# Performance work log

Hardware: AMD Instinct MI355X
Metric: run time of the kernel (lower is better)

## Reference

```python
import jax, jax.numpy as jnp
import numpy as np


def setup_inputs() -> dict:
    key = jax.random.key(0)
    k1, k2, k3, k4 = jax.random.split(key, 4)
    B, S, DIN, DOUT = 4, 4096, 512, 128
    x = jax.random.normal(k1, (B, S, DIN), dtype=jnp.float32)
    Wq = jax.random.normal(k2, (DIN, DOUT), dtype=jnp.float32) * 0.02
    Wk = jax.random.normal(k3, (DIN, DOUT), dtype=jnp.float32) * 0.02
    Wv = jax.random.normal(k4, (DIN, DOUT), dtype=jnp.float32) * 0.02
    return {"x": x, "Wq": Wq, "Wk": Wk, "Wv": Wv}


def reference(x, Wq, Wk, Wv):
    # x: [B, S, d_in]; projections (bias-free Linear)
    q = jnp.einsum('bsd,de->bse', x, Wq)  # [B, S, d_out]
    k = jnp.einsum('bsd,de->bse', x, Wk)
    v = jnp.einsum('bsd,de->bse', x, Wv)
    d_out = k.shape[-1]
    scores = jnp.einsum('bqe,bke->bqk', q, k) / jnp.sqrt(jnp.float32(d_out))  # [B, S, S]
    S = x.shape[1]
    causal = jnp.tril(jnp.ones((S, S), dtype=bool))  # True where attending allowed
    scores = jnp.where(causal[None], scores, jnp.float32(-jnp.inf))
    attn = jax.nn.softmax(scores, axis=-1)
    # dropout p=0.0 -> identity (eval mode)
    return jnp.einsum('bqk,bke->bqe', attn, v)  # [B, S, d_out]
```

## Files before the change

### kernel.cpp

```cpp
#include <hip/hip_runtime.h>

typedef __bf16 bf16x8 __attribute__((ext_vector_type(8)));
typedef float f32x4 __attribute__((ext_vector_type(4)));
typedef unsigned short u16;
typedef unsigned int u32;
typedef u16 u16x8 __attribute__((ext_vector_type(8)));
typedef u16 u16x4 __attribute__((ext_vector_type(4)));
typedef u32 u32x4 __attribute__((ext_vector_type(4)));

__device__ __forceinline__ u16 f2bf(float f) {
    u32 u = __builtin_bit_cast(u32, f);
    u += 0x7fffu + ((u >> 16) & 1u);
    return (u16)(u >> 16);
}
__device__ __forceinline__ float bf2f(u16 v) {
    return __builtin_bit_cast(float, (u32)v << 16);
}
__device__ __forceinline__ u32 cvtpk(float a, float b) {
    u32 d;
    asm("v_cvt_pk_bf16_f32 %0, %1, %2" : "=v"(d) : "v"(a), "v"(b));
    return d;
}
__device__ __forceinline__ f32x4 mfma16(u16x8 a, u16x8 b, f32x4 c) {
    return __builtin_amdgcn_mfma_f32_16x16x32_bf16(
        __builtin_bit_cast(bf16x8, a), __builtin_bit_cast(bf16x8, b), c, 0, 0, 0);
}

#define GLOAD16(SRC, DST)                                                     \
    __builtin_amdgcn_global_load_lds(                                         \
        (const __attribute__((address_space(1))) unsigned int*)(SRC),         \
        (__attribute__((address_space(3))) unsigned int*)(DST), 16, 0, 0)

__device__ __forceinline__ int ldsAddr(int r, int c) {
    return r * 128 + (((c >> 3) ^ (r & 7)) << 3) + (c & 7);
}

__global__ __launch_bounds__(256) void prep_all(
    const float* __restrict__ x,
    const float* __restrict__ Wq, const float* __restrict__ Wk,
    const float* __restrict__ Wv,
    u16* __restrict__ xf, u16* __restrict__ wf)
{
    __shared__ u16 T[16 * 512];
    const int t = threadIdx.x;
    if (blockIdx.x < 1024) {
        const int rb = blockIdx.x;
        const int row = t >> 4, colb = (t & 15) * 32;
        const float* src = x + (size_t)(rb * 16 + row) * 512 + colb;
        #pragma unroll
        for (int i = 0; i < 4; ++i) {
            float4 va = *(const float4*)(src + i * 8);
            float4 vb = *(const float4*)(src + i * 8 + 4);
            u16x8 v;
            v[0] = f2bf(va.x); v[1] = f2bf(va.y); v[2] = f2bf(va.z); v[3] = f2bf(va.w);
            v[4] = f2bf(vb.x); v[5] = f2bf(vb.y); v[6] = f2bf(vb.z); v[7] = f2bf(vb.w);
            int chunk = ((colb >> 3) + i) ^ (row & 7);
            *(u16x8*)&T[row * 512 + chunk * 8] = v;
        }
        __syncthreads();
        #pragma unroll
        for (int ii = 0; ii < 4; ++ii) {
            int flatF = ii * 256 + t;
            int ds = flatF >> 6, lane = flatF & 63;
            int l16 = lane & 15, g = lane >> 4;
            int chunk = (4 * ds + g) ^ (l16 & 7);
            u16x8 v = *(const u16x8*)&T[l16 * 512 + chunk * 8];
            *(u16x8*)&xf[(((size_t)rb * 16 + ds) * 64 + lane) * 8] = v;
        }
    } else {
        int flat = (blockIdx.x - 1024) * 256 + t;
        int widx = flat >> 13, rem = flat & 8191;
        int n = rem >> 10, ds = (rem >> 6) & 15, lane = rem & 63;
        int l16 = lane & 15, g = lane >> 4;
        const float* W = (widx == 0) ? Wq : (widx == 1 ? Wk : Wv);
        const float sc = (widx == 0) ? (0.08838834764831845f * 1.4426950408889634f) : 1.0f;
        u16x8 v;
        #pragma unroll
        for (int j = 0; j < 8; ++j)
            v[j] = f2bf(W[(size_t)(ds * 32 + 8 * g + j) * 128 + n * 16 + l16] * sc);
        *(u16x8*)&wf[(size_t)flat * 8] = v;
    }
}

__global__ __launch_bounds__(256, 3) void qkv2(
    const u16* __restrict__ xf, const u16* __restrict__ wf,
    u16* __restrict__ Qf, u16* __restrict__ Kf, u16* __restrict__ Vf)
{
    __shared__ u16 Wbuf[2][4096];
    __shared__ u16 T4[4][16 * 128];
    const int tid = threadIdx.x, lane = tid & 63, wid = tid >> 6;
    const int g = lane >> 4, l16 = lane & 15;
    const int widx = blockIdx.y;
    const int rbg = blockIdx.x * 4 + wid;
    const u16* WfB = wf + (size_t)widx * 65536;
    u16* T = T4[wid];

    GLOAD16(WfB + (size_t)((wid * 16 + 0) * 64 + lane) * 8,
            Wbuf[0] + (wid * 64 + lane) * 8);
    GLOAD16(WfB + (size_t)(((wid + 4) * 16 + 0) * 64 + lane) * 8,
            Wbuf[0] + ((wid + 4) * 64 + lane) * 8);

    const f32x4 fz = {0.f, 0.f, 0.f, 0.f};
    f32x4 acc[8];
    #pragma unroll
    for (int n = 0; n < 8; ++n) acc[n] = fz;

    u16x8 a_cur = *(const u16x8*)&xf[(((size_t)rbg * 16 + 0) * 64 + lane) * 8];
    __syncthreads();

    #pragma unroll 1
    for (int ds = 0; ds < 16; ++ds) {
        u16x8 a_next;
        if (ds + 1 < 16) {
            const int nds = ds + 1, bb = nds & 1;
            GLOAD16(WfB + (size_t)((wid * 16 + nds) * 64 + lane) * 8,
                    Wbuf[bb] + (wid * 64 + lane) * 8);
            GLOAD16(WfB + (size_t)(((wid + 4) * 16 + nds) * 64 + lane) * 8,
                    Wbuf[bb] + ((wid + 4) * 64 + lane) * 8);
            a_next = *(const u16x8*)&xf[(((size_t)rbg * 16 + nds) * 64 + lane) * 8];
        }
        const u16* Wl = Wbuf[ds & 1];
        #pragma unroll
        for (int n = 0; n < 8; ++n) {
            u16x8 b = *(const u16x8*)&Wl[(n * 64 + lane) * 8];
            acc[n] = mfma16(a_cur, b, acc[n]);
        }
        __syncthreads();
        if (ds + 1 < 16) a_cur = a_next;
    }

    #pragma unroll
    for (int n = 0; n < 8; ++n) {
        #pragma unroll
        for (int r = 0; r < 4; ++r)
            T[ldsAddr(4 * g + r, n * 16 + l16)] = f2bf(acc[n][r]);
    }
    if (widx < 2) {
        u16* dst = (widx == 0) ? Qf : Kf;
        #pragma unroll
        for (int ds = 0; ds < 4; ++ds) {
            int chunk = (4 * ds + g) ^ (l16 & 7);
            u16x8 v = *(const u16x8*)&T[l16 * 128 + chunk * 8];
            *(u16x8*)&dst[(((size_t)rbg * 4 + ds) * 64 + lane) * 8] = v;
        }
    } else {
        const int kb = rbg >> 2, ksel = (rbg >> 1) & 1, g0 = (rbg & 1) * 2;
        #pragma unroll
        for (int s = 0; s < 4; ++s) {
            int flat = s * 64 + lane;
            int e = flat >> 5, gg = (flat >> 4) & 1, l16p = flat & 15;
            u16x8 v;
            #pragma unroll
            for (int j = 0; j < 8; ++j)
                v[j] = T[ldsAddr(8 * gg + j, e * 16 + l16p)];
            *(u16x8*)&Vf[((((size_t)kb * 2 + ksel) * 8 + e) * 64
                          + (g0 + gg) * 16 + l16p) * 8] = v;
        }
    }
}

__global__ __launch_bounds__(256, 2) void attn6(
    const u16* __restrict__ Qf, const u16* __restrict__ Kf,
    const u16* __restrict__ Vf, float* __restrict__ out,
    u16* __restrict__ po, float* __restrict__ pml, int split)
{
    __shared__ u16 lds[2][16384];
    const int tid = threadIdx.x, lane = tid & 63, wid = tid >> 6;
    const int g = lane >> 4, l16 = lane & 15;

    int b, qb, c, u;
    if (split) {
        const int xcd = blockIdx.x & 7;
        b = xcd >> 1;
        int jb = 271 - ((xcd & 1) * 136 + (blockIdx.x >> 3));
        u = 0;
        while ((u + 1) * (u + 2) <= jb) ++u;
        int r = jb - u * (u + 1);
        int hi = (r >= u + 1) ? 1 : 0;
        qb = 2 * u + hi;
        c = r - hi * (u + 1);
    } else {
        b = blockIdx.x & 3;
        qb = blockIdx.x >> 2;
        c = 0; u = 0;
    }
    const int q0 = qb * 128 + wid * 32;
    const int k_lo = c * 256;
    const int k_hi = min(k_lo + (split ? 256 : 4096), qb * 128 + 128);
    const int nch = u + 1;
    const int wklen = q0 + 32;

    {
        const u16* src;
        if (wid < 2) src = Kf + (size_t)(b * 256 + (k_lo >> 4)) * 2048 + wid * 4096;
        else         src = Vf + (size_t)(b * 64 + (k_lo >> 6)) * 8192 + (wid - 2) * 4096;
        u16* dst = &lds[0][wid * 4096];
        #pragma unroll
        for (int j = 0; j < 8; ++j)
            GLOAD16(src + j * 512 + lane * 8, dst + j * 512);
    }
    const int rbq = b * 256 + qb * 8 + wid * 2;
    u16x8 qf0[4], qf1[4];
    #pragma unroll
    for (int ds = 0; ds < 4; ++ds) {
        qf0[ds] = *(const u16x8*)&Qf[(((size_t)rbq * 4 + ds) * 64 + lane) * 8];
        qf1[ds] = *(const u16x8*)&Qf[(((size_t)(rbq + 1) * 4 + ds) * 64 + lane) * 8];
    }

    const f32x4 fz = {0.f, 0.f, 0.f, 0.f};
    f32x4 o0[8], o1[8];
    #pragma unroll
    for (int e = 0; e < 8; ++e) { o0[e] = fz; o1[e] = fz; }
    float l0 = 0.f, l1 = 0.f;

    const int srcA = l16 + ((g & 1) << 5);
    const int srcB = srcA + 16;
    const bool hiSel = (g >= 2);

    __syncthreads();

    int bufsel = 0;
    for (int k0 = k_lo; k0 < k_hi; k0 += 64) {
        if (k0 + 64 < k_hi) {
            const u16* src;
            if (wid < 2) src = Kf + (size_t)(b * 256 + ((k0 + 64) >> 4)) * 2048 + wid * 4096;
            else         src = Vf + (size_t)(b * 64 + ((k0 + 64) >> 6)) * 8192 + (wid - 2) * 4096;
            u16* dst = &lds[bufsel ^ 1][wid * 4096];
            #pragma unroll
            for (int j = 0; j < 8; ++j)
                GLOAD16(src + j * 512 + lane * 8, dst + j * 512);
        }
        if (k0 < wklen) {
            const u16* Kl = &lds[bufsel][0];
            const u16* Vl = &lds[bufsel][8192];
            f32x4 st0[4], st1[4];
            __builtin_amdgcn_s_setprio(1);
            #pragma unroll
            for (int kt = 0; kt < 4; ++kt) {
                st0[kt] = fz; st1[kt] = fz;
                #pragma unroll
                for (int ds = 0; ds < 4; ++ds) {
                    u16x8 kf = *(const u16x8*)&Kl[(kt * 4 + ds) * 512 + lane * 8];
                    st0[kt] = mfma16(kf, qf0[ds], st0[kt]);
                    st1[kt] = mfma16(kf, qf1[ds], st1[kt]);
                }
            }
            __builtin_amdgcn_s_setprio(0);
            if (k0 + 63 > q0) {
                int qg = q0 + l16;
                #pragma unroll
                for (int kt = 0; kt < 4; ++kt)
                    #pragma unroll
                    for (int r = 0; r < 4; ++r)
                        if (k0 + kt * 16 + g * 4 + r > qg) st0[kt][r] = -1e30f;
            }
            if (k0 + 63 > q0 + 16) {
                int qg = q0 + 16 + l16;
                #pragma unroll
                for (int kt = 0; kt < 4; ++kt)
                    #pragma unroll
                    for (int r = 0; r < 4; ++r)
                        if (k0 + kt * 16 + g * 4 + r > qg) st1[kt][r] = -1e30f;
            }
            u32 pk0[4][2], pk1[4][2];
            #pragma unroll
            for (int kt = 0; kt < 4; ++kt) {
                float p0 = exp2f(st0[kt][0]), p1 = exp2f(st0[kt][1]);
                float p2 = exp2f(st0[kt][2]), p3 = exp2f(st0[kt][3]);
                l0 += (p0 + p1) + (p2 + p3);
                pk0[kt][0] = cvtpk(p0, p1);
                pk0[kt][1] = cvtpk(p2, p3);
                float q0v = exp2f(st1[kt][0]), q1v = exp2f(st1[kt][1]);
                float q2v = exp2f(st1[kt][2]), q3v = exp2f(st1[kt][3]);
                l1 += (q0v + q1v) + (q2v + q3v);
                pk1[kt][0] = cvtpk(q0v, q1v);
                pk1[kt][1] = cvtpk(q2v, q3v);
            }
            #pragma unroll
            for (int ksel = 0; ksel < 2; ++ksel) {
                u32 a0 = __shfl((int)pk0[2 * ksel][0], srcA), b0 = __shfl((int)pk0[2 * ksel + 1][0], srcA);
                u32 a1 = __shfl((int)pk0[2 * ksel][1], srcA), b1 = __shfl((int)pk0[2 * ksel + 1][1], srcA);
                u32 a2 = __shfl((int)pk0[2 * ksel][0], srcB), b2 = __shfl((int)pk0[2 * ksel + 1][0], srcB);
                u32 a3 = __shfl((int)pk0[2 * ksel][1], srcB), b3 = __shfl((int)pk0[2 * ksel + 1][1], srcB);
                u32x4 d0 = { hiSel ? b0 : a0, hiSel ? b1 : a1, hiSel ? b2 : a2, hiSel ? b3 : a3 };
                u16x8 pf0 = __builtin_bit_cast(u16x8, d0);
                u32 c0 = __shfl((int)pk1[2 * ksel][0], srcA), e0 = __shfl((int)pk1[2 * ksel + 1][0], srcA);
                u32 c1 = __shfl((int)pk1[2 * ksel][1], srcA), e1 = __shfl((int)pk1[2 * ksel + 1][1], srcA);
                u32 c2 = __shfl((int)pk1[2 * ksel][0], srcB), e2 = __shfl((int)pk1[2 * ksel + 1][0], srcB);
                u32 c3 = __shfl((int)pk1[2 * ksel][1], srcB), e3 = __shfl((int)pk1[2 * ksel + 1][1], srcB);
                u32x4 d1 = { hiSel ? e0 : c0, hiSel ? e1 : c1, hiSel ? e2 : c2, hiSel ? e3 : c3 };
                u16x8 pf1 = __builtin_bit_cast(u16x8, d1);
                __builtin_amdgcn_s_setprio(1);
                #pragma unroll
                for (int e = 0; e < 8; ++e) {
                    u16x8 vf = *(const u16x8*)&Vl[(ksel * 8 + e) * 512 + lane * 8];
                    o0[e] = mfma16(vf, pf0, o0[e]);
                    o1[e] = mfma16(vf, pf1, o1[e]);
                }
                __builtin_amdgcn_s_setprio(0);
            }
        }
        __syncthreads();
        bufsel ^= 1;
    }

    l0 += __shfl_xor(l0, 16); l0 += __shfl_xor(l0, 32);
    l1 += __shfl_xor(l1, 16); l1 += __shfl_xor(l1, 32);

    if (nch == 1) {
        float inv0 = 1.0f / l0, inv1 = 1.0f / l1;
        float* op0 = out + ((size_t)b * 4096 + q0 + l16) * 128;
        float* op1 = out + ((size_t)b * 4096 + q0 + 16 + l16) * 128;
        #pragma unroll
        for (int e = 0; e < 8; ++e) {
            f32x4 v0 = o0[e], v1 = o1[e];
            #pragma unroll
            for (int r = 0; r < 4; ++r) { v0[r] *= inv0; v1[r] *= inv1; }
            *(f32x4*)&op0[e * 16 + g * 4] = v0;
            *(f32x4*)&op1[e * 16 + g * 4] = v1;
        }
    } else {
        const int slot = b * 272 + u * (u + 1) + (qb & 1) * (u + 1) + c;
        u16* pp0 = po + ((size_t)slot * 128 + wid * 32 + l16) * 128;
        u16* pp1 = pp0 + 16 * 128;
        #pragma unroll
        for (int e = 0; e < 8; ++e) {
            u16x4 v0, v1;
            #pragma unroll
            for (int r = 0; r < 4; ++r) { v0[r] = f2bf(o0[e][r]); v1[r] = f2bf(o1[e][r]); }
            *(u16x4*)&pp0[e * 16 + g * 4] = v0;
            *(u16x4*)&pp1[e * 16 + g * 4] = v1;
        }
        if (g == 0) {
            pml[(size_t)slot * 128 + wid * 32 + l16] = l0;
            pml[(size_t)slot * 128 + wid * 32 + 16 + l16] = l1;
        }
    }
}

__global__ __launch_bounds__(256) void merge6(
    const u16* __restrict__ po, const float* __restrict__ pml,
    float* __restrict__ out)
{
    int gid = blockIdx.x * 256 + threadIdx.x;
    int colg = gid & 31;
    int rowid = gid >> 5;
    int b = rowid / 3840;
    int rr = rowid - b * 3840;
    int qb = (rr >> 7) + 2;
    int qr = rr & 127;
    int u = qb >> 1;
    int nch = u + 1;
    int slot0 = b * 272 + u * (u + 1) + (qb & 1) * (u + 1);

    float den = 0.f;
    f32x4 num = {0.f, 0.f, 0.f, 0.f};
    #pragma unroll 1
    for (int cc = 0; cc < nch; ++cc) {
        den += pml[(size_t)(slot0 + cc) * 128 + qr];
        u16x4 pv = *(const u16x4*)&po[((size_t)(slot0 + cc) * 128 + qr) * 128 + colg * 4];
        #pragma unroll
        for (int j = 0; j < 4; ++j) num[j] += bf2f(pv[j]);
    }
    float inv = 1.0f / den;
    f32x4 res = { num[0] * inv, num[1] * inv, num[2] * inv, num[3] * inv };
    *(f32x4*)&out[((size_t)b * 4096 + qb * 128 + qr) * 128 + colg * 4] = res;
}

extern "C" void kernel_launch(void* const* d_in, const int* in_sizes, int n_in,
                              void* d_out, int out_size, void* d_ws, size_t ws_size,
                              hipStream_t stream) {
    (void)in_sizes; (void)n_in; (void)out_size;
    const float* x  = (const float*)d_in[0];
    const float* Wq = (const float*)d_in[1];
    const float* Wk = (const float*)d_in[2];
    const float* Wv = (const float*)d_in[3];
    float* out = (float*)d_out;

    u16* Qf = (u16*)d_ws;
    u16* Kf = Qf + 2097152;
    u16* Vf = Kf + 2097152;
    u16* xf = Vf + 2097152;
    u16* wf = xf + 8388608;
    u16* po = xf;
    float* pml = (float*)(po + (size_t)1088 * 128 * 128);

    const size_t fixed_b = (size_t)3 * 2097152 * 2;
    const size_t part_b  = (size_t)1088 * 128 * (128 * 2 + 4);
    const int split = (ws_size >= fixed_b + part_b) ? 1 : 0;

    prep_all<<<1120, 256, 0, stream>>>(x, Wq, Wk, Wv, xf, wf);
    qkv2<<<dim3(256, 3), 256, 0, stream>>>(xf, wf, Qf, Kf, Vf);
    attn6<<<split ? 1088 : 128, 256, 0, stream>>>(Qf, Kf, Vf, out, po, pml, split);
    if (split) merge6<<<1920, 256, 0, stream>>>(po, pml, out);
}
```

Before: 79.29 us.

## Triple-buffer K/V tiles in attention with two-ahead prefetch and partial vmcnt waits

```diff
diff --git a/kernel.cpp b/kernel.cpp
--- a/kernel.cpp
+++ b/kernel.cpp
@@ -159,14 +159,16 @@
     }
 }
 
-__global__ __launch_bounds__(256, 2) void attn6(
+__global__ __launch_bounds__(256, 2) void attn8(
     const u16* __restrict__ Qf, const u16* __restrict__ Kf,
     const u16* __restrict__ Vf, float* __restrict__ out,
     u16* __restrict__ po, float* __restrict__ pml, int split)
 {
-    __shared__ u16 lds[2][16384];
+    __shared__ u16 lds[3][16384];
+    __shared__ u16 ldspad[8192];
     const int tid = threadIdx.x, lane = tid & 63, wid = tid >> 6;
     const int g = lane >> 4, l16 = lane & 15;
+    if (split == -12345) ldspad[tid] = 0;
 
     int b, qb, c, u;
     if (split) {
@@ -189,15 +191,26 @@
     const int k_hi = min(k_lo + (split ? 256 : 4096), qb * 128 + 128);
     const int nch = u + 1;
     const int wklen = q0 + 32;
+    const int nt = (k_hi - k_lo) >> 6;
 
     {
-        const u16* src;
-        if (wid < 2) src = Kf + (size_t)(b * 256 + (k_lo >> 4)) * 2048 + wid * 4096;
-        else         src = Vf + (size_t)(b * 64 + (k_lo >> 6)) * 8192 + (wid - 2) * 4096;
-        u16* dst = &lds[0][wid * 4096];
+        const u16* src0;
+        if (wid < 2) src0 = Kf + (size_t)(b * 256 + (k_lo >> 4)) * 2048 + wid * 4096;
+        else         src0 = Vf + (size_t)(b * 64 + (k_lo >> 6)) * 8192 + (wid - 2) * 4096;
+        u16* dst0 = &lds[0][wid * 4096];
         #pragma unroll
         for (int j = 0; j < 8; ++j)
-            GLOAD16(src + j * 512 + lane * 8, dst + j * 512);
+            GLOAD16(src0 + j * 512 + lane * 8, dst0 + j * 512);
+        if (nt > 1) {
+            const int k1 = k_lo + 64;
+            const u16* src1;
+            if (wid < 2) src1 = Kf + (size_t)(b * 256 + (k1 >> 4)) * 2048 + wid * 4096;
+            else         src1 = Vf + (size_t)(b * 64 + (k1 >> 6)) * 8192 + (wid - 2) * 4096;
+            u16* dst1 = &lds[1][wid * 4096];
+            #pragma unroll
+            for (int j = 0; j < 8; ++j)
+                GLOAD16(src1 + j * 512 + lane * 8, dst1 + j * 512);
+        }
     }
     const int rbq = b * 256 + qb * 8 + wid * 2;
     u16x8 qf0[4], qf1[4];
@@ -219,20 +232,25 @@
 
     __syncthreads();
 
-    int bufsel = 0;
-    for (int k0 = k_lo; k0 < k_hi; k0 += 64) {
-        if (k0 + 64 < k_hi) {
+    int bi = 0;
+    #pragma unroll 1
+    for (int it = 0; it < nt; ++it) {
+        const int k0 = k_lo + (it << 6);
+        const bool pf = (it + 2 < nt);
+        if (pf) {
+            const int kn = k0 + 128;
+            int pi = bi + 2; if (pi >= 3) pi -= 3;
             const u16* src;
-            if (wid < 2) src = Kf + (size_t)(b * 256 + ((k0 + 64) >> 4)) * 2048 + wid * 4096;
-            else         src = Vf + (size_t)(b * 64 + ((k0 + 64) >> 6)) * 8192 + (wid - 2) * 4096;
-            u16* dst = &lds[bufsel ^ 1][wid * 4096];
+            if (wid < 2) src = Kf + (size_t)(b * 256 + (kn >> 4)) * 2048 + wid * 4096;
+            else         src = Vf + (size_t)(b * 64 + (kn >> 6)) * 8192 + (wid - 2) * 4096;
+            u16* dst = &lds[pi][wid * 4096];
             #pragma unroll
             for (int j = 0; j < 8; ++j)
                 GLOAD16(src + j * 512 + lane * 8, dst + j * 512);
         }
         if (k0 < wklen) {
-            const u16* Kl = &lds[bufsel][0];
-            const u16* Vl = &lds[bufsel][8192];
+            const u16* Kl = &lds[bi][0];
+            const u16* Vl = &lds[bi][8192];
             f32x4 st0[4], st1[4];
             __builtin_amdgcn_s_setprio(1);
             #pragma unroll
@@ -300,8 +318,14 @@
                 __builtin_amdgcn_s_setprio(0);
             }
         }
-        __syncthreads();
-        bufsel ^= 1;
+        if (pf) {
+            asm volatile("s_waitcnt vmcnt(8) lgkmcnt(0)" ::: "memory");
+        } else {
+            asm volatile("s_waitcnt vmcnt(0) lgkmcnt(0)" ::: "memory");
+        }
+        __builtin_amdgcn_s_barrier();
+        __builtin_amdgcn_sched_barrier(0);
+        bi = (bi == 2) ? 0 : bi + 1;
     }
 
     l0 += __shfl_xor(l0, 16); l0 += __shfl_xor(l0, 32);
@@ -391,6 +415,6 @@
 
     prep_all<<<1120, 256, 0, stream>>>(x, Wq, Wk, Wv, xf, wf);
     qkv2<<<dim3(256, 3), 256, 0, stream>>>(xf, wf, Qf, Kf, Vf);
-    attn6<<<split ? 1088 : 128, 256, 0, stream>>>(Qf, Kf, Vf, out, po, pml, split);
+    attn8<<<split ? 1088 : 128, 256, 0, stream>>>(Qf, Kf, Vf, out, po, pml, split);
     if (split) merge6<<<1920, 256, 0, stream>>>(po, pml, out);
 }
```

New measurement: 101.2 us. +27.6%, slower.

## Enlarge attention query tile to 256 rows per block with 64 per wave

Applied to the files above, without the earlier changes.

```diff
diff --git a/kernel.cpp b/kernel.cpp
--- a/kernel.cpp
+++ b/kernel.cpp
@@ -159,7 +159,7 @@
     }
 }
 
-__global__ __launch_bounds__(256, 2) void attn6(
+__global__ __launch_bounds__(256, 2) void attn11(
     const u16* __restrict__ Qf, const u16* __restrict__ Kf,
     const u16* __restrict__ Vf, float* __restrict__ out,
     u16* __restrict__ po, float* __restrict__ pml, int split)
@@ -168,27 +168,29 @@
     const int tid = threadIdx.x, lane = tid & 63, wid = tid >> 6;
     const int g = lane >> 4, l16 = lane & 15;
 
-    int b, qb, c, u;
+    int b, qb, c, nch, slot;
     if (split) {
         const int xcd = blockIdx.x & 7;
         b = xcd >> 1;
-        int jb = 271 - ((xcd & 1) * 136 + (blockIdx.x >> 3));
-        u = 0;
-        while ((u + 1) * (u + 2) <= jb) ++u;
-        int r = jb - u * (u + 1);
-        int hi = (r >= u + 1) ? 1 : 0;
-        qb = 2 * u + hi;
-        c = r - hi * (u + 1);
+        int jb = (xcd & 1) * 68 + (blockIdx.x >> 3);
+        if (jb < 120) {
+            int u = 1;
+            while (u * (u + 1) / 2 <= jb) ++u;
+            qb = u; c = jb - u * (u - 1) / 2;
+        } else {
+            qb = jb - 120; c = qb;
+        }
+        nch = qb + 1;
+        slot = b * 136 + qb * (qb + 1) / 2 + c;
     } else {
         b = blockIdx.x & 3;
         qb = blockIdx.x >> 2;
-        c = 0; u = 0;
-    }
-    const int q0 = qb * 128 + wid * 32;
+        c = 0; nch = 1; slot = 0;
+    }
+    const int q0 = qb * 256 + wid * 64;
     const int k_lo = c * 256;
-    const int k_hi = min(k_lo + (split ? 256 : 4096), qb * 128 + 128);
-    const int nch = u + 1;
-    const int wklen = q0 + 32;
+    const int k_hi = min(k_lo + (split ? 256 : 4096), qb * 256 + 256);
+    const int wklen = q0 + 64;
 
     {
         const u16* src;
@@ -199,19 +201,21 @@
         for (int j = 0; j < 8; ++j)
             GLOAD16(src + j * 512 + lane * 8, dst + j * 512);
     }
-    const int rbq = b * 256 + qb * 8 + wid * 2;
-    u16x8 qf0[4], qf1[4];
+    const int rbq = b * 256 + qb * 16 + wid * 4;
+    u16x8 qf[4][4];
     #pragma unroll
-    for (int ds = 0; ds < 4; ++ds) {
-        qf0[ds] = *(const u16x8*)&Qf[(((size_t)rbq * 4 + ds) * 64 + lane) * 8];
-        qf1[ds] = *(const u16x8*)&Qf[(((size_t)(rbq + 1) * 4 + ds) * 64 + lane) * 8];
-    }
+    for (int h = 0; h < 4; ++h)
+        #pragma unroll
+        for (int ds = 0; ds < 4; ++ds)
+            qf[h][ds] = *(const u16x8*)&Qf[(((size_t)(rbq + h) * 4 + ds) * 64 + lane) * 8];
 
     const f32x4 fz = {0.f, 0.f, 0.f, 0.f};
-    f32x4 o0[8], o1[8];
+    f32x4 o[4][8];
     #pragma unroll
-    for (int e = 0; e < 8; ++e) { o0[e] = fz; o1[e] = fz; }
-    float l0 = 0.f, l1 = 0.f;
+    for (int h = 0; h < 4; ++h)
+        #pragma unroll
+        for (int e = 0; e < 8; ++e) o[h][e] = fz;
+    float l[4] = {0.f, 0.f, 0.f, 0.f};
 
     const int srcA = l16 + ((g & 1) << 5);
     const int srcB = srcA + 16;
@@ -220,6 +224,7 @@
     __syncthreads();
 
     int bufsel = 0;
+    #pragma unroll 1
     for (int k0 = k_lo; k0 < k_hi; k0 += 64) {
         if (k0 + 64 < k_hi) {
             const u16* src;
@@ -233,69 +238,65 @@
         if (k0 < wklen) {
             const u16* Kl = &lds[bufsel][0];
             const u16* Vl = &lds[bufsel][8192];
-            f32x4 st0[4], st1[4];
-            __builtin_amdgcn_s_setprio(1);
-            #pragma unroll
-            for (int kt = 0; kt < 4; ++kt) {
-                st0[kt] = fz; st1[kt] = fz;
+            #pragma unroll
+            for (int ksel = 0; ksel < 2; ++ksel) {
+                u32 pk[4][2][2];
                 #pragma unroll
-                for (int ds = 0; ds < 4; ++ds) {
-                    u16x8 kf = *(const u16x8*)&Kl[(kt * 4 + ds) * 512 + lane * 8];
-                    st0[kt] = mfma16(kf, qf0[ds], st0[kt]);
-                    st1[kt] = mfma16(kf, qf1[ds], st1[kt]);
+                for (int ktl = 0; ktl < 2; ++ktl) {
+                    const int kt = ksel * 2 + ktl;
+                    f32x4 st[4];
+                    __builtin_amdgcn_s_setprio(1);
+                    #pragma unroll
+                    for (int h = 0; h < 4; ++h) st[h] = fz;
+                    #pragma unroll
+                    for (int ds = 0; ds < 4; ++ds) {
+                        u16x8 kf = *(const u16x8*)&Kl[(kt * 4 + ds) * 512 + lane * 8];
+                        #pragma unroll
+                        for (int h = 0; h < 4; ++h)
+                            st[h] = mfma16(kf, qf[h][ds], st[h]);
+                    }
+                    __builtin_amdgcn_s_setprio(0);
+                    #pragma unroll
+                    for (int h = 0; h < 4; ++h) {
+                        if (k0 + kt * 16 + 15 > q0 + h * 16) {
+                            int qg = q0 + h * 16 + l16;
+                            #pragma unroll
+                            for (int r = 0; r < 4; ++r)
+                                if (k0 + kt * 16 + g * 4 + r > qg) st[h][r] = -1e30f;
+                        }
+                    }
+                    #pragma unroll
+                    for (int h = 0; h < 4; ++h) {
+                        float p0 = exp2f(st[h][0]), p1 = exp2f(st[h][1]);
+                        float p2 = exp2f(st[h][2]), p3 = exp2f(st[h][3]);
+                        l[h] += (p0 + p1) + (p2 + p3);
+                        pk[h][ktl][0] = cvtpk(p0, p1);
+                        pk[h][ktl][1] = cvtpk(p2, p3);
+                    }
                 }
-            }
-            __builtin_amdgcn_s_setprio(0);
-            if (k0 + 63 > q0) {
-                int qg = q0 + l16;
-                #pragma unroll
-                for (int kt = 0; kt < 4; ++kt)
+                u16x8 pf0, pf1, pf2, pf3;
+                {
                     #pragma unroll
-                    for (int r = 0; r < 4; ++r)
-                        if (k0 + kt * 16 + g * 4 + r > qg) st0[kt][r] = -1e30f;
-            }
-            if (k0 + 63 > q0 + 16) {
-                int qg = q0 + 16 + l16;
-                #pragma unroll
-                for (int kt = 0; kt < 4; ++kt)
-                    #pragma unroll
-                    for (int r = 0; r < 4; ++r)
-                        if (k0 + kt * 16 + g * 4 + r > qg) st1[kt][r] = -1e30f;
-            }
-            u32 pk0[4][2], pk1[4][2];
-            #pragma unroll
-            for (int kt = 0; kt < 4; ++kt) {
-                float p0 = exp2f(st0[kt][0]), p1 = exp2f(st0[kt][1]);
-                float p2 = exp2f(st0[kt][2]), p3 = exp2f(st0[kt][3]);
-                l0 += (p0 + p1) + (p2 + p3);
-                pk0[kt][0] = cvtpk(p0, p1);
-                pk0[kt][1] = cvtpk(p2, p3);
-                float q0v = exp2f(st1[kt][0]), q1v = exp2f(st1[kt][1]);
-                float q2v = exp2f(st1[kt][2]), q3v = exp2f(st1[kt][3]);
-                l1 += (q0v + q1v) + (q2v + q3v);
-                pk1[kt][0] = cvtpk(q0v, q1v);
-                pk1[kt][1] = cvtpk(q2v, q3v);
-            }
-            #pragma unroll
-            for (int ksel = 0; ksel < 2; ++ksel) {
-                u32 a0 = __shfl((int)pk0[2 * ksel][0], srcA), b0 = __shfl((int)pk0[2 * ksel + 1][0], srcA);
-                u32 a1 = __shfl((int)pk0[2 * ksel][1], srcA), b1 = __shfl((int)pk0[2 * ksel + 1][1], srcA);
-                u32 a2 = __shfl((int)pk0[2 * ksel][0], srcB), b2 = __shfl((int)pk0[2 * ksel + 1][0], srcB);
-                u32 a3 = __shfl((int)pk0[2 * ksel][1], srcB), b3 = __shfl((int)pk0[2 * ksel + 1][1], srcB);
-                u32x4 d0 = { hiSel ? b0 : a0, hiSel ? b1 : a1, hiSel ? b2 : a2, hiSel ? b3 : a3 };
-                u16x8 pf0 = __builtin_bit_cast(u16x8, d0);
-                u32 c0 = __shfl((int)pk1[2 * ksel][0], srcA), e0 = __shfl((int)pk1[2 * ksel + 1][0], srcA);
-                u32 c1 = __shfl((int)pk1[2 * ksel][1], srcA), e1 = __shfl((int)pk1[2 * ksel + 1][1], srcA);
-                u32 c2 = __shfl((int)pk1[2 * ksel][0], srcB), e2 = __shfl((int)pk1[2 * ksel + 1][0], srcB);
-                u32 c3 = __shfl((int)pk1[2 * ksel][1], srcB), e3 = __shfl((int)pk1[2 * ksel + 1][1], srcB);
-                u32x4 d1 = { hiSel ? e0 : c0, hiSel ? e1 : c1, hiSel ? e2 : c2, hiSel ? e3 : c3 };
-                u16x8 pf1 = __builtin_bit_cast(u16x8, d1);
+                    for (int h = 0; h < 4; ++h) {
+                        u32 A0 = __shfl((int)pk[h][0][0], srcA), B0 = __shfl((int)pk[h][1][0], srcA);
+                        u32 A1 = __shfl((int)pk[h][0][1], srcA), B1 = __shfl((int)pk[h][1][1], srcA);
+                        u32 A2 = __shfl((int)pk[h][0][0], srcB), B2 = __shfl((int)pk[h][1][0], srcB);
+                        u32 A3 = __shfl((int)pk[h][0][1], srcB), B3 = __shfl((int)pk[h][1][1], srcB);
+                        u32x4 d = { hiSel ? B0 : A0, hiSel ? B1 : A1,
+                                    hiSel ? B2 : A2, hiSel ? B3 : A3 };
+                        u16x8 pfv = __builtin_bit_cast(u16x8, d);
+                        if (h == 0) pf0 = pfv; else if (h == 1) pf1 = pfv;
+                        else if (h == 2) pf2 = pfv; else pf3 = pfv;
+                    }
+                }
                 __builtin_amdgcn_s_setprio(1);
                 #pragma unroll
                 for (int e = 0; e < 8; ++e) {
                     u16x8 vf = *(const u16x8*)&Vl[(ksel * 8 + e) * 512 + lane * 8];
-                    o0[e] = mfma16(vf, pf0, o0[e]);
-                    o1[e] = mfma16(vf, pf1, o1[e]);
+                    o[0][e] = mfma16(vf, pf0, o[0][e]);
+                    o[1][e] = mfma16(vf, pf1, o[1][e]);
+                    o[2][e] = mfma16(vf, pf2, o[2][e]);
+                    o[3][e] = mfma16(vf, pf3, o[3][e]);
                 }
                 __builtin_amdgcn_s_setprio(0);
             }
@@ -304,41 +305,46 @@
         bufsel ^= 1;
     }
 
-    l0 += __shfl_xor(l0, 16); l0 += __shfl_xor(l0, 32);
-    l1 += __shfl_xor(l1, 16); l1 += __shfl_xor(l1, 32);
+    #pragma unroll
+    for (int h = 0; h < 4; ++h) {
+        l[h] += __shfl_xor(l[h], 16);
+        l[h] += __shfl_xor(l[h], 32);
+    }
 
     if (nch == 1) {
-        float inv0 = 1.0f / l0, inv1 = 1.0f / l1;
-        float* op0 = out + ((size_t)b * 4096 + q0 + l16) * 128;
-        float* op1 = out + ((size_t)b * 4096 + q0 + 16 + l16) * 128;
-        #pragma unroll
-        for (int e = 0; e < 8; ++e) {
-            f32x4 v0 = o0[e], v1 = o1[e];
-            #pragma unroll
-            for (int r = 0; r < 4; ++r) { v0[r] *= inv0; v1[r] *= inv1; }
-            *(f32x4*)&op0[e * 16 + g * 4] = v0;
-            *(f32x4*)&op1[e * 16 + g * 4] = v1;
+        #pragma unroll
+        for (int h = 0; h < 4; ++h) {
+            float inv = 1.0f / l[h];
+            float* op = out + ((size_t)b * 4096 + q0 + h * 16 + l16) * 128;
+            #pragma unroll
+            for (int e = 0; e < 8; ++e) {
+                f32x4 v = o[h][e];
+                #pragma unroll
+                for (int r = 0; r < 4; ++r) v[r] *= inv;
+                *(f32x4*)&op[e * 16 + g * 4] = v;
+            }
         }
     } else {
-        const int slot = b * 272 + u * (u + 1) + (qb & 1) * (u + 1) + c;
-        u16* pp0 = po + ((size_t)slot * 128 + wid * 32 + l16) * 128;
-        u16* pp1 = pp0 + 16 * 128;
-        #pragma unroll
-        for (int e = 0; e < 8; ++e) {
-            u16x4 v0, v1;
-            #pragma unroll
-            for (int r = 0; r < 4; ++r) { v0[r] = f2bf(o0[e][r]); v1[r] = f2bf(o1[e][r]); }
-            *(u16x4*)&pp0[e * 16 + g * 4] = v0;
-            *(u16x4*)&pp1[e * 16 + g * 4] = v1;
+        #pragma unroll
+        for (int h = 0; h < 4; ++h) {
+            u16* pp = po + ((size_t)slot * 256 + wid * 64 + h * 16 + l16) * 128;
+            #pragma unroll
+            for (int e = 0; e < 8; ++e) {
+                u16x4 v;
+                #pragma unroll
+                for (int r = 0; r < 4; ++r) v[r] = f2bf(o[h][e][r]);
+                *(u16x4*)&pp[e * 16 + g * 4] = v;
+            }
         }
         if (g == 0) {
-            pml[(size_t)slot * 128 + wid * 32 + l16] = l0;
-            pml[(size_t)slot * 128 + wid * 32 + 16 + l16] = l1;
-        }
-    }
-}
-
-__global__ __launch_bounds__(256) void merge6(
+            #pragma unroll
+            for (int h = 0; h < 4; ++h)
+                pml[(size_t)slot * 256 + wid * 64 + h * 16 + l16] = l[h];
+        }
+    }
+}
+
+__global__ __launch_bounds__(256) void merge7(
     const u16* __restrict__ po, const float* __restrict__ pml,
     float* __restrict__ out)
 {
@@ -347,24 +353,23 @@
     int rowid = gid >> 5;
     int b = rowid / 3840;
     int rr = rowid - b * 3840;
-    int qb = (rr >> 7) + 2;
-    int qr = rr & 127;
-    int u = qb >> 1;
-    int nch = u + 1;
-    int slot0 = b * 272 + u * (u + 1) + (qb & 1) * (u + 1);
+    int qb = (rr >> 8) + 1;
+    int qr = rr & 255;
+    int nch = qb + 1;
+    int slot0 = b * 136 + qb * (qb + 1) / 2;
 
     float den = 0.f;
     f32x4 num = {0.f, 0.f, 0.f, 0.f};
     #pragma unroll 1
     for (int cc = 0; cc < nch; ++cc) {
-        den += pml[(size_t)(slot0 + cc) * 128 + qr];
-        u16x4 pv = *(const u16x4*)&po[((size_t)(slot0 + cc) * 128 + qr) * 128 + colg * 4];
+        den += pml[(size_t)(slot0 + cc) * 256 + qr];
+        u16x4 pv = *(const u16x4*)&po[((size_t)(slot0 + cc) * 256 + qr) * 128 + colg * 4];
         #pragma unroll
         for (int j = 0; j < 4; ++j) num[j] += bf2f(pv[j]);
     }
     float inv = 1.0f / den;
     f32x4 res = { num[0] * inv, num[1] * inv, num[2] * inv, num[3] * inv };
-    *(f32x4*)&out[((size_t)b * 4096 + qb * 128 + qr) * 128 + colg * 4] = res;
+    *(f32x4*)&out[((size_t)b * 4096 + qb * 256 + qr) * 128 + colg * 4] = res;
 }
 
 extern "C" void kernel_launch(void* const* d_in, const int* in_sizes, int n_in,
@@ -383,14 +388,14 @@
     u16* xf = Vf + 2097152;
     u16* wf = xf + 8388608;
     u16* po = xf;
-    float* pml = (float*)(po + (size_t)1088 * 128 * 128);
+    float* pml = (float*)(po + (size_t)544 * 256 * 128);
 
     const size_t fixed_b = (size_t)3 * 2097152 * 2;
-    const size_t part_b  = (size_t)1088 * 128 * (128 * 2 + 4);
+    const size_t part_b  = (size_t)544 * 256 * (128 * 2 + 4);
     const int split = (ws_size >= fixed_b + part_b) ? 1 : 0;
 
     prep_all<<<1120, 256, 0, stream>>>(x, Wq, Wk, Wv, xf, wf);
     qkv2<<<dim3(256, 3), 256, 0, stream>>>(xf, wf, Qf, Kf, Vf);
-    attn6<<<split ? 1088 : 128, 256, 0, stream>>>(Qf, Kf, Vf, out, po, pml, split);
-    if (split) merge6<<<1920, 256, 0, stream>>>(po, pml, out);
-}
+    attn11<<<split ? 544 : 64, 256, 0, stream>>>(Qf, Kf, Vf, out, po, pml, split);
+    if (split) merge7<<<1920, 256, 0, stream>>>(po, pml, out);
+}
```

After: 139.6 us. +76.1%, slower.
